# Kernel tuning notes

Measured on AMD Instinct MI355X. Metric: run time of the kernel, lower is better.

Reference implementation:

```python
import jax, jax.numpy as jnp
import numpy as np

B, K_LEN, Q_LEN, E, H = 16, 2048, 1024, 512, 8


def _layer_norm(x, g, b, eps=1e-5):
    mu = jnp.mean(x, axis=-1, keepdims=True)
    var = jnp.mean(jnp.square(x - mu), axis=-1, keepdims=True)
    return (x - mu) * jax.lax.rsqrt(var + eps) * g + b


def setup_inputs() -> dict:
    key = jax.random.key(0)
    ks = jax.random.split(key, 8)
    w = lambda k, sh: (jax.random.normal(k, sh, dtype=jnp.float32) * 0.02)
    return {
        "x_key": jax.random.normal(ks[0], (B, K_LEN, E), dtype=jnp.float32),
        "in_proj_w": w(ks[1], (3 * E, E)),
        "in_proj_b": jnp.zeros((3 * E,), jnp.float32),
        "out_w": w(ks[2], (E, E)),
        "out_b": jnp.zeros((E,), jnp.float32),
        "ln1_g": jnp.ones((E,), jnp.float32),
        "ln1_b": jnp.zeros((E,), jnp.float32),
        "w1": w(ks[3], (E, E)),
        "b1": jnp.zeros((E,), jnp.float32),
        "w2": w(ks[4], (E, E)),
        "b2": jnp.zeros((E,), jnp.float32),
        "ln2_g": jnp.ones((E,), jnp.float32),
        "ln2_b": jnp.zeros((E,), jnp.float32),
        "query_length": Q_LEN,
        "key_padding_mask": jax.random.bernoulli(ks[5], 0.2, (B, K_LEN)),
    }


def _attn_mask(key_length, query_length, key_padding_mask):
    # True = masked.  triu causal part, shared across batch/heads.
    triu = jnp.triu(jnp.ones((key_length, key_length), dtype=bool), k=1)
    m = triu[-query_length:]  # [Q, K]
    m = m[None] | key_padding_mask[:, None, :]  # [B, Q, K]
    not_eye = ~jnp.eye(key_length, dtype=bool)[-query_length:]  # [Q, K]
    m = m & not_eye[None]  # diagonal (self) always attendable
    return m  # [B, Q, K]; identical across heads


def reference(x_key, in_proj_w, in_proj_b, out_w, out_b,
              ln1_g, ln1_b, w1, b1, w2, b2, ln2_g, ln2_b,
              query_length, key_padding_mask):
    b, k_len, e = x_key.shape
    dh = e // H
    q_len = query_length

    # pad key_padding_mask on the left with its first column (static shapes)
    L = key_padding_mask.shape[1]
    if L < k_len:
        pad = jnp.repeat(key_padding_mask[:, :1], k_len - L, axis=1)
        key_padding_mask = jnp.concatenate([pad, key_padding_mask], axis=1)

    query = x_key[:, -q_len:]  # [B, Q, E]

    wq, wk, wv = jnp.split(in_proj_w, 3, axis=0)
    bq, bk, bv = jnp.split(in_proj_b, 3, axis=0)
    q = (query @ wq.T + bq).reshape(b, q_len, H, dh).transpose(0, 2, 1, 3)
    k = (x_key @ wk.T + bk).reshape(b, k_len, H, dh).transpose(0, 2, 1, 3)
    v = (x_key @ wv.T + bv).reshape(b, k_len, H, dh).transpose(0, 2, 1, 3)

    scores = jnp.einsum('bhqd,bhkd->bhqk', q, k) * (dh ** -0.5)
    mask = _attn_mask(k_len, q_len, key_padding_mask)  # [B, Q, K]
    scores = jnp.where(mask[:, None], -jnp.inf, scores)
    attn = jax.nn.softmax(scores, axis=-1)  # [B, H, Q, K]

    ctx = jnp.einsum('bhqk,bhkd->bhqd', attn, v)
    ctx = ctx.transpose(0, 2, 1, 3).reshape(b, q_len, e)
    attn_out = ctx @ out_w.T + out_b

    t = _layer_norm(attn_out + query, ln1_g, ln1_b)
    ff = jax.nn.relu(t @ w1.T + b1) @ w2.T + b2
    output = _layer_norm(ff + t, ln2_g, ln2_b)
    attn_weights = attn.mean(axis=1)  # head-averaged, torch default
    return output, attn_weights
```

## Files before the change

### kernel.cpp

```cpp
#include <hip/hip_runtime.h>

typedef unsigned short u16t;
typedef __attribute__((ext_vector_type(4))) unsigned short us4;
typedef __attribute__((ext_vector_type(8))) unsigned short us8;
typedef __attribute__((ext_vector_type(8))) short s8v;
typedef __attribute__((ext_vector_type(4))) float f4v;

#define NB 16
#define KL 2048
#define QL 1024
#define EE 512
#define NH 8
#define DH 64

#define QSCALE 0.18033688011112042f

__device__ __forceinline__ float b2f(u16t u) {
  return __uint_as_float(((unsigned)u) << 16);
}
__device__ __forceinline__ u16t f2b(float f) {
  unsigned u = __float_as_uint(f);
  u += 0x7fffu + ((u >> 16) & 1u);
  return (u16t)(u >> 16);
}
__device__ __forceinline__ u16t f2b_fast(float f) {
  return (u16t)((__float_as_uint(f) + 0x8000u) >> 16);
}
__device__ __forceinline__ float fexp2(float x) {
  return __builtin_amdgcn_exp2f(x);
}

__device__ __forceinline__ int detect_mode(const int* kpm_i) {
  bool small = true, oddzero = true, evenone = false;
  for (int i = 0; i < 64; ++i) {
    unsigned v = (unsigned)kpm_i[i];
    if (v > 1u) small = false;
    if ((i & 1) && v != 0u) oddzero = false;
    if (!(i & 1) && v == 1u) evenone = true;
  }
  return !small ? 0 : ((oddzero && evenone) ? 2 : 1);
}

__global__ __launch_bounds__(256) void cvt_weights(
    const float* __restrict__ wi, const float* __restrict__ wo,
    const float* __restrict__ wf1, const float* __restrict__ wf2,
    u16t* __restrict__ dst) {
  int i = blockIdx.x * 256 + threadIdx.x;
  const float* src;
  int j;
  if (i < 196608) { src = wi; j = i; }
  else if (i < 262144) { src = wo; j = i - 196608; }
  else if (i < 327680) { src = wf1; j = i - 262144; }
  else { src = wf2; j = i - 327680; }
  float4 v = ((const float4*)src)[j];
  us4 o = {f2b(v.x), f2b(v.y), f2b(v.z), f2b(v.w)};
  *(us4*)&dst[i * 4] = o;
}

__global__ __launch_bounds__(256) void mfma_gemm_qkv(
    const float* __restrict__ A, const u16t* __restrict__ Wb,
    const float* __restrict__ bias, u16t* __restrict__ q_ws,
    u16t* __restrict__ k_ws, u16t* __restrict__ v_ws) {
  const int Kd = EE;
  __shared__ u16t Alds[128 * 40];
  __shared__ u16t Blds[128 * 40];
  const int t = threadIdx.x;
  const int n0 = blockIdx.x * 128, m0 = blockIdx.y * 128;
  const int lane = t & 63, w = t >> 6;
  const int col = lane & 15, quad = lane >> 4;
  const int wm = w & 1, wn = w >> 1;

  const int arow = t >> 1, ahalf = t & 1;
  const int wrow = t >> 1, wseg = t & 1;

  f4v acc[4][4] = {};

  for (int kc = 0; kc < Kd; kc += 32) {
    const float* ap = &A[(size_t)(m0 + arow) * Kd + kc + ahalf * 16];
    float4 f0 = ((const float4*)ap)[0];
    float4 f1 = ((const float4*)ap)[1];
    float4 f2_ = ((const float4*)ap)[2];
    float4 f3 = ((const float4*)ap)[3];
    const u16t* wp = &Wb[(size_t)(n0 + wrow) * Kd + kc + wseg * 16];
    us8 w0 = *(const us8*)wp;
    us8 w1 = *(const us8*)(wp + 8);
    __syncthreads();
    us8 o0 = {f2b(f0.x), f2b(f0.y), f2b(f0.z), f2b(f0.w),
              f2b(f1.x), f2b(f1.y), f2b(f1.z), f2b(f1.w)};
    us8 o1 = {f2b(f2_.x), f2b(f2_.y), f2b(f2_.z), f2b(f2_.w),
              f2b(f3.x), f2b(f3.y), f2b(f3.z), f2b(f3.w)};
    *(us8*)&Alds[arow * 40 + ahalf * 16] = o0;
    *(us8*)&Alds[arow * 40 + ahalf * 16 + 8] = o1;
    *(us8*)&Blds[wrow * 40 + wseg * 16] = w0;
    *(us8*)&Blds[wrow * 40 + wseg * 16 + 8] = w1;
    __syncthreads();
    s8v af[4], bf[4];
#pragma unroll
    for (int mt = 0; mt < 4; ++mt)
      af[mt] = *(s8v*)&Alds[(wm * 64 + mt * 16 + col) * 40 + quad * 8];
#pragma unroll
    for (int nt = 0; nt < 4; ++nt)
      bf[nt] = *(s8v*)&Blds[(wn * 64 + nt * 16 + col) * 40 + quad * 8];
#pragma unroll
    for (int mt = 0; mt < 4; ++mt)
#pragma unroll
      for (int nt = 0; nt < 4; ++nt)
        acc[mt][nt] = __builtin_amdgcn_mfma_f32_16x16x32_bf16(
            af[mt], bf[nt], acc[mt][nt], 0, 0, 0);
  }

  float bv[4];
#pragma unroll
  for (int nt = 0; nt < 4; ++nt) bv[nt] = bias[n0 + wn * 64 + nt * 16 + col];

#pragma unroll
  for (int nt = 0; nt < 4; ++nt) {
    int n = n0 + wn * 64 + nt * 16 + col;
    int sec = n >> 9, hh = (n >> 6) & 7, dd = n & 63;
#pragma unroll
    for (int mt = 0; mt < 4; ++mt)
#pragma unroll
      for (int r = 0; r < 4; ++r) {
        int m = m0 + wm * 64 + mt * 16 + quad * 4 + r;
        int bb_ = m >> 11, pos = m & 2047;
        u16t o = f2b(acc[mt][nt][r] + bv[nt]);
        if (sec == 0) {
          if (pos >= QL) q_ws[((bb_ * NH + hh) * QL + pos - QL) * DH + dd] = o;
        } else if (sec == 1) {
          k_ws[((bb_ * NH + hh) * KL + pos) * DH + dd] = o;
        } else {
          v_ws[((bb_ * NH + hh) * DH + dd) * KL + pos] = o;
        }
      }
  }
}

__global__ __launch_bounds__(256) void mfma_gemm_bias(
    const u16t* __restrict__ A, const u16t* __restrict__ Wb,
    const float* __restrict__ bias, u16t* __restrict__ C, int M, int N,
    int Kd, int relu) {
  __shared__ u16t Alds[128 * 40];
  __shared__ u16t Blds[128 * 40];
  const int t = threadIdx.x;
  const int n0 = blockIdx.x * 128, m0 = blockIdx.y * 128;
  const int lane = t & 63, w = t >> 6;
  const int col = lane & 15, quad = lane >> 4;
  const int wm = w & 1, wn = w >> 1;
  const int row = t >> 1, seg = t & 1;

  f4v acc[4][4] = {};

  for (int kc = 0; kc < Kd; kc += 32) {
    const u16t* ap = &A[(size_t)(m0 + row) * Kd + kc + seg * 16];
    us8 a0 = *(const us8*)ap;
    us8 a1 = *(const us8*)(ap + 8);
    const u16t* wp = &Wb[(size_t)(n0 + row) * Kd + kc + seg * 16];
    us8 w0 = *(const us8*)wp;
    us8 w1 = *(const us8*)(wp + 8);
    __syncthreads();
    *(us8*)&Alds[row * 40 + seg * 16] = a0;
    *(us8*)&Alds[row * 40 + seg * 16 + 8] = a1;
    *(us8*)&Blds[row * 40 + seg * 16] = w0;
    *(us8*)&Blds[row * 40 + seg * 16 + 8] = w1;
    __syncthreads();
    s8v af[4], bf[4];
#pragma unroll
    for (int mt = 0; mt < 4; ++mt)
      af[mt] = *(s8v*)&Alds[(wm * 64 + mt * 16 + col) * 40 + quad * 8];
#pragma unroll
    for (int nt = 0; nt < 4; ++nt)
      bf[nt] = *(s8v*)&Blds[(wn * 64 + nt * 16 + col) * 40 + quad * 8];
#pragma unroll
    for (int mt = 0; mt < 4; ++mt)
#pragma unroll
      for (int nt = 0; nt < 4; ++nt)
        acc[mt][nt] = __builtin_amdgcn_mfma_f32_16x16x32_bf16(
            af[mt], bf[nt], acc[mt][nt], 0, 0, 0);
  }

  float bv[4];
#pragma unroll
  for (int nt = 0; nt < 4; ++nt) bv[nt] = bias[n0 + wn * 64 + nt * 16 + col];

#pragma unroll
  for (int mt = 0; mt < 4; ++mt)
#pragma unroll
    for (int nt = 0; nt < 4; ++nt) {
      int n = n0 + wn * 64 + nt * 16 + col;
#pragma unroll
      for (int r = 0; r < 4; ++r) {
        int m = m0 + wm * 64 + mt * 16 + quad * 4 + r;
        float v = acc[mt][nt][r] + bv[nt];
        if (relu) v = fmaxf(v, 0.f);
        C[(size_t)m * N + n] = f2b(v);
      }
    }
}

__global__ __launch_bounds__(256, 2) void attn_fwd(
    const u16t* __restrict__ qw, const u16t* __restrict__ kw,
    const u16t* __restrict__ vw, const int* kpm_i, const unsigned char* kpm_b,
    u16t* __restrict__ ctx_out, float* __restrict__ m_ws,
    float* __restrict__ l_ws) {
  const int q0 = blockIdx.x * 32;
  const int bh = blockIdx.y;
  const int b = bh >> 3, h = bh & 7;
  const int t = threadIdx.x;
  const int lane = t & 63, w = t >> 6;
  const int col = lane & 15, quad = lane >> 4;

  __shared__ unsigned char padb[KL];
  __shared__ __align__(16) char ubuf[32768];
  u16t (*plds)[2][16][72] = (u16t (*)[2][16][72])ubuf;
  float (*ctxm)[32][64] = (float (*)[32][64])ubuf;
  __shared__ float mlm[4][2][32];
  __shared__ float Lrow[32], ewf[4][32];
  __shared__ int mode_s;

  if (t == 0) mode_s = detect_mode(kpm_i);
  __syncthreads();
  const int mode = mode_s;
  for (int i = t; i < KL; i += 256) {
    int idx = b * KL + i;
    padb[i] = (mode == 0)
                  ? (kpm_b[idx] != 0)
                  : (mode == 1 ? (kpm_i[idx] != 0) : (kpm_i[2 * idx] != 0));
  }
  __syncthreads();

  s8v qa[2][2];
#pragma unroll
  for (int st = 0; st < 2; ++st)
#pragma unroll
    for (int hf = 0; hf < 2; ++hf)
      qa[st][hf] = *(const s8v*)&qw[(bh * QL + q0 + st * 16 + col) * DH +
                                    quad * 8 + 32 * hf];

  f4v cacc[2][4];
#pragma unroll
  for (int st = 0; st < 2; ++st)
#pragma unroll
    for (int dt = 0; dt < 4; ++dt) cacc[st][dt] = (f4v){0.f, 0.f, 0.f, 0.f};
  float mr[2][4], lr[2][4];
#pragma unroll
  for (int st = 0; st < 2; ++st)
#pragma unroll
    for (int r = 0; r < 4; ++r) { mr[st][r] = -1.0e30f; lr[st][r] = 0.f; }

  const int qmaxk = q0 + 31 + QL;
  const f4v zf = {0.f, 0.f, 0.f, 0.f};
  const size_t kbase = (size_t)bh * KL * DH;
  const size_t vbase = (size_t)bh * DH * KL;

  int kc = w * 64;
  s8v kcur[4][2];
#pragma unroll
  for (int tt = 0; tt < 4; ++tt) {
    const u16t* kp = &kw[kbase + (size_t)(kc + tt * 16 + col) * DH + quad * 8];
    kcur[tt][0] = *(const s8v*)kp;
    kcur[tt][1] = *(const s8v*)(kp + 32);
  }

  while (true) {
    s8v vcur[4][2];
#pragma unroll
    for (int dt = 0; dt < 4; ++dt) {
      const u16t* vp = &vw[vbase + (size_t)(dt * 16 + col) * KL + kc + quad * 8];
      vcur[dt][0] = *(const s8v*)vp;
      vcur[dt][1] = *(const s8v*)(vp + 32);
    }
    const int kcn = kc + 256;
    const bool more = (kcn <= qmaxk);
    s8v knxt[4][2];
    if (more) {
#pragma unroll
      for (int tt = 0; tt < 4; ++tt) {
        const u16t* kp =
            &kw[kbase + (size_t)(kcn + tt * 16 + col) * DH + quad * 8];
        knxt[tt][0] = *(const s8v*)kp;
        knxt[tt][1] = *(const s8v*)(kp + 32);
      }
    }

    f4v sts[2][4];
#pragma unroll
    for (int tt = 0; tt < 4; ++tt)
#pragma unroll
      for (int st = 0; st < 2; ++st) {
        f4v c = __builtin_amdgcn_mfma_f32_16x16x32_bf16(qa[st][0],
                                                        kcur[tt][0], zf, 0, 0, 0);
        sts[st][tt] = __builtin_amdgcn_mfma_f32_16x16x32_bf16(
            qa[st][1], kcur[tt][1], c, 0, 0, 0);
      }

    const bool interior = (kc + 63 < q0 + QL);

#pragma unroll
    for (int st = 0; st < 2; ++st) {
      float cmax[4] = {-1.0e30f, -1.0e30f, -1.0e30f, -1.0e30f};
      if (interior) {
#pragma unroll
        for (int tt = 0; tt < 4; ++tt) {
          bool pad = padb[kc + tt * 16 + col] != 0;
#pragma unroll
          for (int r = 0; r < 4; ++r) {
            float v = pad ? -1.0e30f : sts[st][tt][r] * QSCALE;
            sts[st][tt][r] = v;
            cmax[r] = fmaxf(cmax[r], v);
          }
        }
      } else {
#pragma unroll
        for (int tt = 0; tt < 4; ++tt) {
          int key = kc + tt * 16 + col;
          bool pad = padb[key] != 0;
#pragma unroll
          for (int r = 0; r < 4; ++r) {
            int qrow = q0 + st * 16 + quad * 4 + r;
            bool al = (key <= qrow + QL) && (!pad || key == qrow + QL);
            float v = al ? sts[st][tt][r] * QSCALE : -1.0e30f;
            sts[st][tt][r] = v;
            cmax[r] = fmaxf(cmax[r], v);
          }
        }
      }
#pragma unroll
      for (int mk = 1; mk < 16; mk <<= 1)
#pragma unroll
        for (int r = 0; r < 4; ++r)
          cmax[r] = fmaxf(cmax[r], __shfl_xor(cmax[r], mk, 16));
      float alpha[4], rsum[4];
#pragma unroll
      for (int r = 0; r < 4; ++r) {
        float mn = fmaxf(mr[st][r], cmax[r]);
        alpha[r] = fexp2(mr[st][r] - mn);
        mr[st][r] = mn;
        rsum[r] = 0.f;
      }
#pragma unroll
      for (int tt = 0; tt < 4; ++tt)
#pragma unroll
        for (int r = 0; r < 4; ++r) {
          float v = sts[st][tt][r];
          float p = (v > -1.0e29f) ? fexp2(v - mr[st][r]) : 0.f;
          sts[st][tt][r] = p;
          rsum[r] += p;
        }
#pragma unroll
      for (int mk = 1; mk < 16; mk <<= 1)
#pragma unroll
        for (int r = 0; r < 4; ++r) rsum[r] += __shfl_xor(rsum[r], mk, 16);
#pragma unroll
      for (int r = 0; r < 4; ++r) {
        lr[st][r] = lr[st][r] * alpha[r] + rsum[r];
#pragma unroll
        for (int dt = 0; dt < 4; ++dt) cacc[st][dt][r] *= alpha[r];
      }
#pragma unroll
      for (int tt = 0; tt < 4; ++tt)
#pragma unroll
        for (int r = 0; r < 4; ++r)
          plds[w][st][quad * 4 + r][tt * 16 + col] = f2b_fast(sts[st][tt][r]);
    }

    s8v pa[2][2];
#pragma unroll
    for (int st = 0; st < 2; ++st)
#pragma unroll
      for (int hf = 0; hf < 2; ++hf)
        pa[st][hf] = *(const s8v*)&plds[w][st][col][hf * 32 + quad * 8];
#pragma unroll
    for (int dt = 0; dt < 4; ++dt)
#pragma unroll
      for (int st = 0; st < 2; ++st) {
        cacc[st][dt] = __builtin_amdgcn_mfma_f32_16x16x32_bf16(
            pa[st][0], vcur[dt][0], cacc[st][dt], 0, 0, 0);
        cacc[st][dt] = __builtin_amdgcn_mfma_f32_16x16x32_bf16(
            pa[st][1], vcur[dt][1], cacc[st][dt], 0, 0, 0);
      }

    if (!more) break;
    kc = kcn;
#pragma unroll
    for (int tt = 0; tt < 4; ++tt) {
      kcur[tt][0] = knxt[tt][0];
      kcur[tt][1] = knxt[tt][1];
    }
  }

  __syncthreads();
#pragma unroll
  for (int st = 0; st < 2; ++st)
#pragma unroll
    for (int dt = 0; dt < 4; ++dt)
#pragma unroll
      for (int r = 0; r < 4; ++r)
        ctxm[w][st * 16 + quad * 4 + r][dt * 16 + col] = cacc[st][dt][r];
  if (col == 0) {
#pragma unroll
    for (int st = 0; st < 2; ++st)
#pragma unroll
      for (int r = 0; r < 4; ++r) {
        mlm[w][0][st * 16 + quad * 4 + r] = mr[st][r];
        mlm[w][1][st * 16 + quad * 4 + r] = lr[st][r];
      }
  }
  __syncthreads();
  if (t < 32) {
    int q = t;
    float M = mlm[0][0][q];
#pragma unroll
    for (int ww = 1; ww < 4; ++ww) M = fmaxf(M, mlm[ww][0][q]);
    float L = 0.f;
#pragma unroll
    for (int ww = 0; ww < 4; ++ww) {
      float e = fexp2(mlm[ww][0][q] - M);
      ewf[ww][q] = e;
      L += mlm[ww][1][q] * e;
    }
    Lrow[q] = 1.0f / L;
    m_ws[bh * QL + q0 + q] = M;
    l_ws[bh * QL + q0 + q] = L;
  }
  __syncthreads();
  for (int i = t; i < 2048; i += 256) {
    int q = i >> 6, d = i & 63;
    float v = ctxm[0][q][d] * ewf[0][q] + ctxm[1][q][d] * ewf[1][q] +
              ctxm[2][q][d] * ewf[2][q] + ctxm[3][q][d] * ewf[3][q];
    v *= Lrow[q];
    ctx_out[(b * QL + q0 + q) * EE + h * DH + d] = f2b(v);
  }
}

__global__ __launch_bounds__(256) void attn_aw(
    const u16t* __restrict__ qw, const u16t* __restrict__ kw,
    const int* kpm_i, const unsigned char* kpm_b,
    const float* __restrict__ m_ws, const float* __restrict__ l_ws,
    float* __restrict__ aw_out) {
  const int q0 = blockIdx.x * 32;
  const int k0 = blockIdx.y * 128;
  const int b = blockIdx.z;
  const int t = threadIdx.x;
  const int lane = t & 63, w = t >> 6;
  const int col = lane & 15, quad = lane >> 4;
  const int qmaxk = q0 + 31 + QL;

  if (k0 > qmaxk) {
    for (int i = t; i < 32 * 128; i += 256) {
      int q = i >> 7, c = i & 127;
      aw_out[(b * QL + q0 + q) * KL + k0 + c] = 0.f;
    }
    return;
  }

  __shared__ unsigned char padb[128];
  __shared__ int mode_s;
  if (t == 0) mode_s = detect_mode(kpm_i);
  __syncthreads();
  const int mode = mode_s;
  if (t < 128) {
    int idx = b * KL + k0 + t;
    padb[t] = (mode == 0)
                  ? (kpm_b[idx] != 0)
                  : (mode == 1 ? (kpm_i[idx] != 0) : (kpm_i[2 * idx] != 0));
  }
  __syncthreads();

  const bool interior = (k0 + 127 < q0 + QL);

  const int kt = k0 + w * 32;
  const f4v zf = {0.f, 0.f, 0.f, 0.f};
  f4v acc[2][2];
#pragma unroll
  for (int st = 0; st < 2; ++st)
#pragma unroll
    for (int tt = 0; tt < 2; ++tt) acc[st][tt] = zf;

  for (int h = 0; h < NH; ++h) {
    const int bh = b * NH + h;
    s8v qa[2][2];
#pragma unroll
    for (int st = 0; st < 2; ++st)
#pragma unroll
      for (int hf = 0; hf < 2; ++hf)
        qa[st][hf] = *(const s8v*)&qw[(bh * QL + q0 + st * 16 + col) * DH +
                                      quad * 8 + 32 * hf];
    float Mv[2][4], Li[2][4];
#pragma unroll
    for (int st = 0; st < 2; ++st)
#pragma unroll
      for (int r = 0; r < 4; ++r) {
        int q = q0 + st * 16 + quad * 4 + r;
        Mv[st][r] = m_ws[bh * QL + q];
        Li[st][r] = 1.0f / l_ws[bh * QL + q];
      }
#pragma unroll
    for (int tt = 0; tt < 2; ++tt) {
      const int ktt = kt + tt * 16;
      if (ktt > qmaxk) continue;
      const u16t* kp = &kw[(bh * KL + ktt + col) * DH + quad * 8];
      s8v kb0 = *(const s8v*)kp;
      s8v kb1 = *(const s8v*)(kp + 32);
      int key = ktt + col;
      bool pad = padb[key - k0] != 0;
#pragma unroll
      for (int st = 0; st < 2; ++st) {
        f4v c = __builtin_amdgcn_mfma_f32_16x16x32_bf16(qa[st][0], kb0, zf, 0, 0, 0);
        c = __builtin_amdgcn_mfma_f32_16x16x32_bf16(qa[st][1], kb1, c, 0, 0, 0);
        if (interior) {
#pragma unroll
          for (int r = 0; r < 4; ++r) {
            float p = pad ? 0.f
                          : fexp2(c[r] * QSCALE - Mv[st][r]) * Li[st][r];
            acc[st][tt][r] += 0.125f * p;
          }
        } else {
#pragma unroll
          for (int r = 0; r < 4; ++r) {
            int qrow = q0 + st * 16 + quad * 4 + r;
            bool al = (key <= qrow + QL) && (!pad || key == qrow + QL);
            float p = al ? fexp2(c[r] * QSCALE - Mv[st][r]) * Li[st][r] : 0.f;
            acc[st][tt][r] += 0.125f * p;
          }
        }
      }
    }
  }
#pragma unroll
  for (int st = 0; st < 2; ++st)
#pragma unroll
    for (int tt = 0; tt < 2; ++tt)
#pragma unroll
      for (int r = 0; r < 4; ++r)
        aw_out[(b * QL + q0 + st * 16 + quad * 4 + r) * KL + kt + tt * 16 +
               col] = acc[st][tt][r];
}

__global__ __launch_bounds__(256) void ln_res(
    const u16t* __restrict__ x, const u16t* __restrict__ res_b,
    const float* __restrict__ res_f, int res_is_xkey,
    const float* __restrict__ g, const float* __restrict__ bb,
    u16t* __restrict__ out_b, float* __restrict__ out_f, int out_f32) {
  __shared__ float red[4];
  int row = blockIdx.x;
  int t = threadIdx.x;
  int base = row * EE;
  float r0, r1;
  if (res_is_xkey) {
    int b = row >> 10, qq = row & 1023;
    int rbase = (b * KL + QL + qq) * EE;
    r0 = res_f[rbase + t];
    r1 = res_f[rbase + t + 256];
  } else {
    r0 = b2f(res_b[base + t]);
    r1 = b2f(res_b[base + t + 256]);
  }
  float a0 = b2f(x[base + t]) + r0;
  float a1 = b2f(x[base + t + 256]) + r1;
  float sv = a0 + a1;
#pragma unroll
  for (int off = 32; off > 0; off >>= 1) sv += __shfl_down(sv, off);
  if ((t & 63) == 0) red[t >> 6] = sv;
  __syncthreads();
  float mu = (red[0] + red[1] + red[2] + red[3]) * (1.0f / 512.0f);
  __syncthreads();
  float d0 = a0 - mu, d1 = a1 - mu;
  float vv = d0 * d0 + d1 * d1;
#pragma unroll
  for (int off = 32; off > 0; off >>= 1) vv += __shfl_down(vv, off);
  if ((t & 63) == 0) red[t >> 6] = vv;
  __syncthreads();
  float var = (red[0] + red[1] + red[2] + red[3]) * (1.0f / 512.0f);
  float rs = rsqrtf(fmaxf(var, 0.f) + 1e-5f);
  float o0 = d0 * rs * g[t] + bb[t];
  float o1 = d1 * rs * g[t + 256] + bb[t + 256];
  if (out_f32) {
    out_f[base + t] = o0;
    out_f[base + t + 256] = o1;
  } else {
    out_b[base + t] = f2b(o0);
    out_b[base + t + 256] = f2b(o1);
  }
}

extern "C" void kernel_launch(void* const* d_in, const int* in_sizes, int n_in,
                              void* d_out, int out_size, void* d_ws,
                              size_t ws_size, hipStream_t stream) {
  const float* x_key = (const float*)d_in[0];
  const float* in_proj_w = (const float*)d_in[1];
  const float* in_proj_b = (const float*)d_in[2];
  const float* out_w = (const float*)d_in[3];
  const float* out_b = (const float*)d_in[4];
  const float* ln1_g = (const float*)d_in[5];
  const float* ln1_b = (const float*)d_in[6];
  const float* w1 = (const float*)d_in[7];
  const float* b1 = (const float*)d_in[8];
  const float* w2 = (const float*)d_in[9];
  const float* b2 = (const float*)d_in[10];
  const float* ln2_g = (const float*)d_in[11];
  const float* ln2_b = (const float*)d_in[12];
  const void* kpm = d_in[14];

  float* out = (float*)d_out;
  u16t* ws = (u16t*)d_ws;

  u16t* wb_inproj = ws;
  u16t* wb_out = ws + 786432;
  u16t* wb_w1 = ws + 1048576;
  u16t* wb_w2 = ws + 1310720;
  u16t* q_ws = ws + 1572864;
  u16t* k_ws = ws + 9961472;
  u16t* v_ws = ws + 26738688;
  u16t* ctx_ws = ws + 43515904;
  float* m_ws = (float*)(ws + 51904512);
  float* l_ws = m_ws + 131072;
  u16t* ao_ws = q_ws;
  u16t* t_ws = ctx_ws;
  u16t* h1_ws = k_ws;
  u16t* ff_ws = v_ws;
  float* aw_out = out + (NB * QL * EE);

  cvt_weights<<<1536, 256, 0, stream>>>(in_proj_w, out_w, w1, w2, wb_inproj);
  mfma_gemm_qkv<<<dim3(12, 256), 256, 0, stream>>>(x_key, wb_inproj,
                                                   in_proj_b, q_ws, k_ws,
                                                   v_ws);
  attn_fwd<<<dim3(QL / 32, NB * NH), 256, 0, stream>>>(
      q_ws, k_ws, v_ws, (const int*)kpm, (const unsigned char*)kpm, ctx_ws,
      m_ws, l_ws);
  attn_aw<<<dim3(QL / 32, KL / 128, NB), 256, 0, stream>>>(
      q_ws, k_ws, (const int*)kpm, (const unsigned char*)kpm, m_ws, l_ws,
      aw_out);
  mfma_gemm_bias<<<dim3(4, 128), 256, 0, stream>>>(ctx_ws, wb_out, out_b,
                                                   ao_ws, NB * QL, EE, EE, 0);
  ln_res<<<NB * QL, 256, 0, stream>>>(ao_ws, nullptr, x_key, 1, ln1_g, ln1_b,
                                      t_ws, nullptr, 0);
  mfma_gemm_bias<<<dim3(4, 128), 256, 0, stream>>>(t_ws, wb_w1, b1, h1_ws,
                                                   NB * QL, EE, EE, 1);
  mfma_gemm_bias<<<dim3(4, 128), 256, 0, stream>>>(h1_ws, wb_w2, b2, ff_ws,
                                                   NB * QL, EE, EE, 0);
  ln_res<<<NB * QL, 256, 0, stream>>>(ff_ws, t_ws, nullptr, 0, ln2_g, ln2_b,
                                      nullptr, out, 1);
}
```

Before: 1.012 ms.

## Fold softmax scale into Q projection and compute row sums via MFMA

After: 974.5 us. 1.04x faster.

```diff
diff --git a/kernel.cpp b/kernel.cpp
--- a/kernel.cpp
+++ b/kernel.cpp
@@ -14,6 +14,7 @@
 #define DH 64
 
 #define QSCALE 0.18033688011112042f
+#define SENT (-60000.0f)
 
 __device__ __forceinline__ float b2f(u16t u) {
   return __uint_as_float(((unsigned)u) << 16);
@@ -123,13 +124,15 @@
       for (int r = 0; r < 4; ++r) {
         int m = m0 + wm * 64 + mt * 16 + quad * 4 + r;
         int bb_ = m >> 11, pos = m & 2047;
-        u16t o = f2b(acc[mt][nt][r] + bv[nt]);
+        float val = acc[mt][nt][r] + bv[nt];
         if (sec == 0) {
-          if (pos >= QL) q_ws[((bb_ * NH + hh) * QL + pos - QL) * DH + dd] = o;
+          if (pos >= QL)
+            q_ws[((bb_ * NH + hh) * QL + pos - QL) * DH + dd] =
+                f2b(val * QSCALE);
         } else if (sec == 1) {
-          k_ws[((bb_ * NH + hh) * KL + pos) * DH + dd] = o;
+          k_ws[((bb_ * NH + hh) * KL + pos) * DH + dd] = f2b(val);
         } else {
-          v_ws[((bb_ * NH + hh) * DH + dd) * KL + pos] = o;
+          v_ws[((bb_ * NH + hh) * DH + dd) * KL + pos] = f2b(val);
         }
       }
   }
@@ -236,19 +239,25 @@
       qa[st][hf] = *(const s8v*)&qw[(bh * QL + q0 + st * 16 + col) * DH +
                                     quad * 8 + 32 * hf];
 
+  const f4v zf = {0.f, 0.f, 0.f, 0.f};
+  const s8v ones = {16256, 16256, 16256, 16256,
+                    16256, 16256, 16256, 16256};
+
   f4v cacc[2][4];
+  f4v lacc[2];
+#pragma unroll
+  for (int st = 0; st < 2; ++st) {
+    lacc[st] = zf;
+#pragma unroll
+    for (int dt = 0; dt < 4; ++dt) cacc[st][dt] = zf;
+  }
+  float mr[2][4];
 #pragma unroll
   for (int st = 0; st < 2; ++st)
 #pragma unroll
-    for (int dt = 0; dt < 4; ++dt) cacc[st][dt] = (f4v){0.f, 0.f, 0.f, 0.f};
-  float mr[2][4], lr[2][4];
-#pragma unroll
-  for (int st = 0; st < 2; ++st)
-#pragma unroll
-    for (int r = 0; r < 4; ++r) { mr[st][r] = -1.0e30f; lr[st][r] = 0.f; }
+    for (int r = 0; r < 4; ++r) mr[st][r] = SENT;
 
   const int qmaxk = q0 + 31 + QL;
-  const f4v zf = {0.f, 0.f, 0.f, 0.f};
   const size_t kbase = (size_t)bh * KL * DH;
   const size_t vbase = (size_t)bh * DH * KL;
 
@@ -297,14 +306,14 @@
 
 #pragma unroll
     for (int st = 0; st < 2; ++st) {
-      float cmax[4] = {-1.0e30f, -1.0e30f, -1.0e30f, -1.0e30f};
+      float cmax[4] = {SENT, SENT, SENT, SENT};
       if (interior) {
 #pragma unroll
         for (int tt = 0; tt < 4; ++tt) {
           bool pad = padb[kc + tt * 16 + col] != 0;
 #pragma unroll
           for (int r = 0; r < 4; ++r) {
-            float v = pad ? -1.0e30f : sts[st][tt][r] * QSCALE;
+            float v = pad ? -1.0e30f : sts[st][tt][r];
             sts[st][tt][r] = v;
             cmax[r] = fmaxf(cmax[r], v);
           }
@@ -318,7 +327,7 @@
           for (int r = 0; r < 4; ++r) {
             int qrow = q0 + st * 16 + quad * 4 + r;
             bool al = (key <= qrow + QL) && (!pad || key == qrow + QL);
-            float v = al ? sts[st][tt][r] * QSCALE : -1.0e30f;
+            float v = al ? sts[st][tt][r] : -1.0e30f;
             sts[st][tt][r] = v;
             cmax[r] = fmaxf(cmax[r], v);
           }
@@ -329,38 +338,26 @@
 #pragma unroll
         for (int r = 0; r < 4; ++r)
           cmax[r] = fmaxf(cmax[r], __shfl_xor(cmax[r], mk, 16));
-      float alpha[4], rsum[4];
+      float alpha[4];
 #pragma unroll
       for (int r = 0; r < 4; ++r) {
         float mn = fmaxf(mr[st][r], cmax[r]);
         alpha[r] = fexp2(mr[st][r] - mn);
         mr[st][r] = mn;
-        rsum[r] = 0.f;
+      }
+#pragma unroll
+      for (int r = 0; r < 4; ++r) {
+        lacc[st][r] *= alpha[r];
+#pragma unroll
+        for (int dt = 0; dt < 4; ++dt) cacc[st][dt][r] *= alpha[r];
       }
 #pragma unroll
       for (int tt = 0; tt < 4; ++tt)
 #pragma unroll
         for (int r = 0; r < 4; ++r) {
-          float v = sts[st][tt][r];
-          float p = (v > -1.0e29f) ? fexp2(v - mr[st][r]) : 0.f;
-          sts[st][tt][r] = p;
-          rsum[r] += p;
+          float p = fexp2(sts[st][tt][r] - mr[st][r]);
+          plds[w][st][quad * 4 + r][tt * 16 + col] = f2b_fast(p);
         }
-#pragma unroll
-      for (int mk = 1; mk < 16; mk <<= 1)
-#pragma unroll
-        for (int r = 0; r < 4; ++r) rsum[r] += __shfl_xor(rsum[r], mk, 16);
-#pragma unroll
-      for (int r = 0; r < 4; ++r) {
-        lr[st][r] = lr[st][r] * alpha[r] + rsum[r];
-#pragma unroll
-        for (int dt = 0; dt < 4; ++dt) cacc[st][dt][r] *= alpha[r];
-      }
-#pragma unroll
-      for (int tt = 0; tt < 4; ++tt)
-#pragma unroll
-        for (int r = 0; r < 4; ++r)
-          plds[w][st][quad * 4 + r][tt * 16 + col] = f2b_fast(sts[st][tt][r]);
     }
 
     s8v pa[2][2];
@@ -369,6 +366,13 @@
 #pragma unroll
       for (int hf = 0; hf < 2; ++hf)
         pa[st][hf] = *(const s8v*)&plds[w][st][col][hf * 32 + quad * 8];
+#pragma unroll
+    for (int st = 0; st < 2; ++st) {
+      lacc[st] = __builtin_amdgcn_mfma_f32_16x16x32_bf16(pa[st][0], ones,
+                                                         lacc[st], 0, 0, 0);
+      lacc[st] = __builtin_amdgcn_mfma_f32_16x16x32_bf16(pa[st][1], ones,
+                                                         lacc[st], 0, 0, 0);
+    }
 #pragma unroll
     for (int dt = 0; dt < 4; ++dt)
 #pragma unroll
@@ -402,7 +406,7 @@
 #pragma unroll
       for (int r = 0; r < 4; ++r) {
         mlm[w][0][st * 16 + quad * 4 + r] = mr[st][r];
-        mlm[w][1][st * 16 + quad * 4 + r] = lr[st][r];
+        mlm[w][1][st * 16 + quad * 4 + r] = lacc[st][r];
       }
   }
   __syncthreads();
@@ -510,8 +514,7 @@
         if (interior) {
 #pragma unroll
           for (int r = 0; r < 4; ++r) {
-            float p = pad ? 0.f
-                          : fexp2(c[r] * QSCALE - Mv[st][r]) * Li[st][r];
+            float p = pad ? 0.f : fexp2(c[r] - Mv[st][r]) * Li[st][r];
             acc[st][tt][r] += 0.125f * p;
           }
         } else {
@@ -519,7 +522,7 @@
           for (int r = 0; r < 4; ++r) {
             int qrow = q0 + st * 16 + quad * 4 + r;
             bool al = (key <= qrow + QL) && (!pad || key == qrow + QL);
-            float p = al ? fexp2(c[r] * QSCALE - Mv[st][r]) * Li[st][r] : 0.f;
+            float p = al ? fexp2(c[r] - Mv[st][r]) * Li[st][r] : 0.f;
             acc[st][tt][r] += 0.125f * p;
           }
         }
```
